# Optimization experiments

Hardware: AMD Instinct MI355X
Metric: run time of the kernel (lower is better)

Reference implementation:

```python
import jax, jax.numpy as jnp
import numpy as np

DET_COUNT = 729
N_ANGLES = 90
IMG = 512
FEATURES = 32
FILTER_SIZE = max(64, int(2 ** np.ceil(np.log2(2 * DET_COUNT))))  # 2048


def _ramp_filter(size):
    # scikit-image / torch_radon style spatial-domain ram-lak, then FFT
    n = np.concatenate([np.arange(1, size // 2 + 1, 2), np.arange(size // 2 - 1, 0, -2)])
    f = np.zeros(size, dtype=np.float64)
    f[0] = 0.25
    f[1::2] = -1.0 / (np.pi * n) ** 2
    return jnp.asarray(2.0 * np.real(np.fft.fft(f)), dtype=jnp.float32)

_RAMP = _ramp_filter(FILTER_SIZE)


def radon_forward(img, theta, det_count):
    # parallel-beam line integrals; img: (B, C, n, n)
    B, C, n, _ = img.shape
    c = (n - 1) / 2.0
    s = jnp.arange(det_count, dtype=img.dtype) - (det_count - 1) / 2.0  # detector offsets == ray steps
    cos, sin = jnp.cos(theta), jnp.sin(theta)
    # sample points: p = c + s*dir_perp + t*dir_ray   -> coords (A, D, T)
    px = c + s[None, :, None] * cos[:, None, None] - s[None, None, :] * sin[:, None, None]
    py = c + s[None, :, None] * sin[:, None, None] + s[None, None, :] * cos[:, None, None]

    def sample(im2d):
        vals = jax.scipy.ndimage.map_coordinates(im2d, [py, px], order=1, mode='constant', cval=0.0)
        return vals.sum(-1)  # integrate along ray -> (A, D)

    sino = jax.vmap(sample)(img.reshape(B * C, n, n))
    return sino.reshape(B, C, theta.shape[0], det_count)


def filter_sinogram(sino, n_angles):
    det = sino.shape[-1]
    padded = jnp.pad(sino, ((0, 0), (0, 0), (0, 0), (0, FILTER_SIZE - det)))
    out = jnp.real(jnp.fft.ifft(jnp.fft.fft(padded, axis=-1) * _RAMP, axis=-1))[..., :det]
    return out * (jnp.pi / (2.0 * n_angles))


def radon_backprojection(sino, theta, n):
    B, C, A, D = sino.shape
    c = (n - 1) / 2.0
    xs = jnp.arange(n, dtype=sino.dtype) - c
    X = xs[None, :]  # columns -> x
    Y = xs[:, None]  # rows    -> y
    cos, sin = jnp.cos(theta), jnp.sin(theta)
    pos = X[None] * cos[:, None, None] + Y[None] * sin[:, None, None] + (D - 1) / 2.0  # (A, n, n)
    i0 = jnp.clip(jnp.floor(pos), 0, D - 2).astype(jnp.int32)
    w = pos - i0
    valid = (pos >= 0) & (pos <= D - 1)

    def back_one(sino_ad):  # (A, D) -> (n, n)
        def per_angle(row, idx, ww, vv):
            v = row[idx] * (1.0 - ww) + row[idx + 1] * ww
            return jnp.where(vv, v, 0.0)
        return jax.vmap(per_angle)(sino_ad, i0, w, valid).sum(0)

    return jax.vmap(back_one)(sino.reshape(B * C, A, D)).reshape(B, C, n, n)


def conv2d(x, w):
    return jax.lax.conv_general_dilated(x, w, (1, 1), 'SAME', dimension_numbers=('NCHW', 'OIHW', 'NCHW'))


def setup_inputs():
    key = jax.random.key(0)
    ks = jax.random.split(key, 10)

    def xavier(k, shape):
        fan_in = shape[1] * shape[2] * shape[3]
        fan_out = shape[0] * shape[2] * shape[3]
        std = float(np.sqrt(2.0 / (fan_in + fan_out)))
        return jax.random.normal(k, shape, dtype=jnp.float32) * std

    x = jax.random.normal(ks[0], (1, 1, IMG, IMG), dtype=jnp.float32)
    theta = jnp.linspace(0.0, np.pi, N_ANGLES, endpoint=False).astype(jnp.float32)
    sinogram = jax.random.normal(ks[1], (1, 1, N_ANGLES, DET_COUNT), dtype=jnp.float32)
    return {
        'x': x, 'theta': theta, 'sinogram': sinogram,
        'lambda_step': jnp.asarray([0.5], dtype=jnp.float32),
        'soft_thr': jnp.asarray([0.01], dtype=jnp.float32),
        'conv_D': xavier(ks[2], (FEATURES, 1, 3, 3)),
        'conv1_forward': xavier(ks[3], (FEATURES, FEATURES, 3, 3)),
        'conv2_forward': xavier(ks[4], (FEATURES, FEATURES, 3, 3)),
        'conv1_backward': xavier(ks[5], (FEATURES, FEATURES, 3, 3)),
        'conv2_backward': xavier(ks[6], (FEATURES, FEATURES, 3, 3)),
        'conv_G': xavier(ks[7], (1, FEATURES, 3, 3)),
    }


def reference(x, theta, sinogram, lambda_step, soft_thr, conv_D, conv1_forward, conv2_forward, conv1_backward, conv2_backward, conv_G):
    sino_pred = radon_forward(x, theta, DET_COUNT)
    filtered = filter_sinogram(sino_pred, theta.shape[0])
    X_fbp = radon_backprojection(filtered - sinogram, theta, x.shape[2])
    x_input = x - lambda_step[0] * X_fbp

    x_D = conv2d(x_input, conv_D)
    h = jax.nn.relu(conv2d(x_D, conv1_forward))
    x_forward = conv2d(h, conv2_forward)
    st = jnp.sign(x_forward) * jax.nn.relu(jnp.abs(x_forward) - soft_thr[0])
    h = jax.nn.relu(conv2d(st, conv1_backward))
    x_backward = conv2d(h, conv2_backward)
    x_G = conv2d(x_backward, conv_G)
    x_pred = x_input + x_G

    h = jax.nn.relu(conv2d(x_forward, conv1_backward))
    x_D_est = conv2d(h, conv2_backward)
    symloss = x_D_est - x_D
    return (x_pred, symloss, symloss)
```

## Files before the change

### kernel.cpp

```cpp
#include <hip/hip_runtime.h>

#define IMG   512
#define NA    90
#define DET   729
#define NPIX  (IMG*IMG)
#define HW    514
#define QW    514
#define HBELEMS (HW*HW*32)

typedef __attribute__((ext_vector_type(8))) short     bf16x8;
typedef __attribute__((ext_vector_type(8))) unsigned short ushort8;
typedef __attribute__((ext_vector_type(4))) float     f32x4;

__device__ __forceinline__ unsigned short f2b(float f) {
    unsigned int u = __builtin_bit_cast(unsigned int, f);
    return (unsigned short)((u + 0x7FFFu + ((u >> 16) & 1u)) >> 16);
}
__device__ __forceinline__ float b2f(unsigned short h) {
    return __builtin_bit_cast(float, (unsigned int)h << 16);
}

__global__ void prep0_k(const float* __restrict__ theta, const float* __restrict__ img,
                        float* __restrict__ trig, float4* __restrict__ quad4,
                        float* __restrict__ sino) {
    if (blockIdx.x == 0) {
        int i = threadIdx.x;
        if (i < NA) {
            float t = theta[i];
            trig[2*i]   = cosf(t);
            trig[2*i+1] = sinf(t);
        }
        return;
    }
    if (blockIdx.x <= 1033) {
        int q = (blockIdx.x - 1) * 256 + threadIdx.x;
        if (q >= QW*QW) return;
        int qy = q / QW, qx = q - qy*QW;
        auto val = [&](int r, int c) -> float {
            return (r >= 1 && r <= 512 && c >= 1 && c <= 512) ? img[((r-1) << 9) + (c-1)] : 0.f;
        };
        quad4[q] = make_float4(val(qy, qx), val(qy, qx+1), val(qy+1, qx), val(qy+1, qx+1));
        return;
    }
    int z = (blockIdx.x - 1034) * 256 + threadIdx.x;
    if (z < NA*DET) sino[z] = 0.f;
}

__global__ __launch_bounds__(256) void radon_tile_k(const float4* __restrict__ quad4,
        const float* __restrict__ trig, float* __restrict__ sino) {
    __shared__ float4 tl4[1226];
    int b  = blockIdx.x;
    int tq = b % 289;
    int g  = b / 289;
    int tx = tq % 17, ty = tq / 17;
    int X0 = tx*32, Y0 = ty*32;
    int tid = threadIdx.x;

    for (int e = tid; e < 1226; e += 256) {
        float4 v = make_float4(0.f, 0.f, 0.f, 0.f);
        int r = e / 35, c = e - r*35;
        if (r >= 1 && r <= 32 && c >= 1 && c <= 32) {
            int gy = Y0 + r - 1, gx = X0 + c - 1;
            if (gy < QW && gx < QW) v = quad4[gy*QW + gx];
        }
        tl4[e] = v;
    }
    __syncthreads();

    int w = tid >> 6, lane = tid & 63;
    int a = g*4 + w;
    if (a >= NA) return;
    float cs = trig[2*a], sn = trig[2*a+1];

    float fX0 = (float)X0 - 1.0f;
    float fY0 = (float)Y0 - 1.0f;

    float cx0 = fX0 - 255.5f, cx1 = cx0 + 32.0f;
    float cy0 = fY0 - 255.5f, cy1 = cy0 + 32.0f;
    float sdmin = fminf(cx0*cs, cx1*cs) + fminf(cy0*sn, cy1*sn);
    float sdmax = fmaxf(cx0*cs, cx1*cs) + fmaxf(cy0*sn, cy1*sn);
    int dmin = (int)ceilf(sdmin + 364.0f) - 1; if (dmin < 0) dmin = 0;
    int dmax = (int)floorf(sdmax + 364.0f) + 1; if (dmax > DET-1) dmax = DET-1;
    int d = dmin + lane;
    if (d > dmax) return;

    float sd = (float)d - 364.0f;
    float bx = 255.5f + sd*cs, by = 255.5f + sd*sn;
    float lo = -365.0f, hi = 365.0f;
    if (sn > 1e-7f) {
        float inv = 1.0f / sn;
        lo = (bx - (fX0 + 32.0f)) * inv;
        hi = (bx - fX0) * inv;
    } else if (bx < fX0 || bx >= fX0 + 32.0f) return;
    if (fabsf(cs) > 1e-7f) {
        float inv = 1.0f / cs;
        float s1 = (fY0 - by) * inv, s2 = (fY0 + 32.0f - by) * inv;
        lo = fmaxf(lo, fminf(s1, s2));
        hi = fminf(hi, fmaxf(s1, s2));
    } else if (by < fY0 || by >= fY0 + 32.0f) return;
    int jlo = (int)ceilf(lo + 364.0f) - 1; if (jlo < 0) jlo = 0;
    int jhi = (int)floorf(hi + 364.0f) + 1; if (jhi > DET-1) jhi = DET-1;
    if (jlo > jhi) return;

    float sj = (float)jlo - 364.0f;
    float px2 = bx - sj*sn - fX0 + 1.0f;
    float py2 = by + sj*cs - fY0 + 1.0f;
    float acc = 0.f;
    #pragma unroll 2
    for (int j = jlo; j <= jhi; ++j) {
        float fpx = floorf(px2), fpy = floorf(py2);
        int ix = (int)fpx, iy = (int)fpy;
        float fx = px2 - fpx, fy = py2 - fpy;
        unsigned ba = ((unsigned)(iy*35 + ix)) * 16u;
        if (ba > 19584u) ba = 19600u;
        float4 q = *(const float4*)((const char*)tl4 + ba);
        float top = fmaf(fx, q.y - q.x, q.x);
        float bot = fmaf(fx, q.w - q.z, q.z);
        acc += fmaf(fy, bot - top, top);
        px2 -= sn; py2 += cs;
    }
    if (acc != 0.f) atomicAdd(&sino[a*DET + d], acc);
}

__global__ __launch_bounds__(768) void filter_k(const float* __restrict__ sino,
        const float* __restrict__ meas, float2* __restrict__ dpair) {
    __shared__ float prow[DET + 2*728];
    __shared__ float invsq[364];
    __shared__ float drow[DET];
    int a = blockIdx.x;
    for (int t = threadIdx.x; t < DET + 2*728; t += 768)
        prow[t] = (t >= 728 && t < 728 + DET) ? sino[a*DET + (t - 728)] : 0.f;
    const float cc = -2.0f / (3.14159265358979323846f * 3.14159265358979323846f);
    if (threadIdx.x < 364) {
        float dlt = (float)(2*threadIdx.x + 1);
        invsq[threadIdx.x] = cc / (dlt * dlt);
    }
    __syncthreads();
    const float scale = 3.14159265358979323846f / 180.0f;
    int i = threadIdx.x;
    if (i < DET) {
        const float* p = prow + 728 + i;
        float acc = 0.5f * p[0];
        #pragma unroll 4
        for (int k = 0; k < 364; k++) {
            int dlt = 2*k + 1;
            acc += (p[-dlt] + p[dlt]) * invsq[k];
        }
        drow[i] = acc * scale - meas[a*DET + i];
    }
    __syncthreads();
    if (i < DET)
        dpair[a*DET + i] = make_float2(drow[i], (i < DET-1) ? drow[i+1] : 0.f);
}

__global__ __launch_bounds__(256) void backproj_k(const float2* __restrict__ pair,
        const float* __restrict__ trig, const float* __restrict__ x,
        const float* __restrict__ lam, float* __restrict__ xin) {
    int pix = blockIdx.x * 256 + threadIdx.x;
    float X = (float)(pix & 511) - 255.5f;
    float Y = (float)(pix >> 9) - 255.5f;
    float acc = 0.f;
    for (int a = 0; a < NA; a++) {
        float pos = X*trig[2*a] + Y*trig[2*a+1] + 364.0f;
        if (pos >= 0.f && pos <= 728.f) {
            int i0 = (int)pos;
            if (i0 > 727) i0 = 727;
            float w = pos - (float)i0;
            float2 p = pair[a*DET + i0];
            acc += p.x + w*(p.y - p.x);
        }
    }
    xin[pix] = x[pix] - lam[0] * acc;
}

__global__ void prep1_k(unsigned short* __restrict__ hb0, size_t hbstride_elems,
                        const float* __restrict__ w0, const float* __restrict__ w1,
                        const float* __restrict__ w2, const float* __restrict__ w3,
                        const float* __restrict__ wg4,
                        unsigned short* __restrict__ wbuf) {
    int t = blockIdx.x * 256 + threadIdx.x;
    if (t < 4*2052) {
        int b = t / 2052, r = t - b*2052;
        int py, px;
        if      (r < 514)  { py = 0;            px = r; }
        else if (r < 1028) { py = 513;          px = r - 514; }
        else if (r < 1540) { py = r - 1028 + 1; px = 0; }
        else               { py = r - 1540 + 1; px = 513; }
        unsigned short* p = hb0 + b*hbstride_elems + ((size_t)py*HW + px)*32;
        uint4 z = make_uint4(0,0,0,0);
        ((uint4*)p)[0] = z; ((uint4*)p)[1] = z; ((uint4*)p)[2] = z; ((uint4*)p)[3] = z;
        return;
    }
    int tid = t - 4*2052;
    if (tid < 4*9216) {
        int L = tid / 9216, r = tid - L*9216;
        int tt = r >> 10, o = (r >> 5) & 31, i = r & 31;
        const float* s = (L == 0) ? w0 : (L == 1) ? w1 : (L == 2) ? w2 : w3;
        wbuf[tid] = f2b(s[o*288 + i*9 + tt]);
        return;
    }
    int gid = tid - 4*9216;
    if (gid >= 9*512) return;
    int tt = gid / 512, r = gid - tt*512;
    int o = r >> 5, i = r & 31;
    wbuf[4*9216 + gid] = (o == 0) ? f2b(wg4[i*9 + tt]) : (unsigned short)0;
}

__global__ __launch_bounds__(256) void convD_k(const float* __restrict__ xin,
        const float* __restrict__ wD, unsigned short* __restrict__ out_nhwc) {
    int pix = blockIdx.x * 256 + threadIdx.x;
    int y = pix >> 9, x = pix & 511;
    float v[9];
    #pragma unroll
    for (int dy = -1; dy <= 1; dy++)
        #pragma unroll
        for (int dx = -1; dx <= 1; dx++) {
            int yy = y + dy, xx = x + dx;
            v[(dy+1)*3 + dx+1] = (yy >= 0 && yy < 512 && xx >= 0 && xx < 512)
                                 ? xin[(yy << 9) + xx] : 0.f;
        }
    unsigned int packed[16];
    #pragma unroll
    for (int oc = 0; oc < 32; ++oc) {
        float acc = 0.f;
        #pragma unroll
        for (int t = 0; t < 9; t++) acc = fmaf(v[t], wD[oc*9 + t], acc);
        unsigned int b = f2b(acc);
        if (oc & 1) packed[oc >> 1] |= b << 16; else packed[oc >> 1] = b;
    }
    uint4* dst = (uint4*)(out_nhwc + ((size_t)(y+1)*HW + (x+1))*32);
    dst[0] = make_uint4(packed[0],  packed[1],  packed[2],  packed[3]);
    dst[1] = make_uint4(packed[4],  packed[5],  packed[6],  packed[7]);
    dst[2] = make_uint4(packed[8],  packed[9],  packed[10], packed[11]);
    dst[3] = make_uint4(packed[12], packed[13], packed[14], packed[15]);
}

template<int MODE>
__global__ __launch_bounds__(256, 4) void convM_k(const unsigned short* __restrict__ in,
        const unsigned short* __restrict__ wb,
        unsigned short* __restrict__ out0, unsigned short* __restrict__ out1,
        const float* __restrict__ thr_p,
        const unsigned short* __restrict__ aux, float* __restrict__ s1, float* __restrict__ s2) {
    int wv   = threadIdx.x >> 6;
    int lane = threadIdx.x & 63;
    int blk  = blockIdx.x;
    int xcd  = blk & 7;
    int idx  = blk >> 3;
    int by = (xcd << 2) + (idx >> 5);
    int bx = idx & 31;
    int x0 = bx*16;
    int yb = by*16 + wv*4;
    int lpix = lane & 15;
    int k8   = (lane >> 4) * 8;

    f32x4 acc[2][4];
    #pragma unroll
    for (int ob = 0; ob < 2; ob++)
        #pragma unroll
        for (int o = 0; o < 4; o++) acc[ob][o] = (f32x4){0.f,0.f,0.f,0.f};

    const short* base = (const short*)in + ((size_t)yb*HW + (x0 + lpix))*32 + k8;

    #pragma unroll
    for (int dx = 0; dx < 3; ++dx) {
        bf16x8 A2[3][2];
        #pragma unroll
        for (int dy = 0; dy < 3; ++dy)
            #pragma unroll
            for (int ob = 0; ob < 2; ob++)
                A2[dy][ob] = *(const bf16x8*)(wb + (dy*3+dx)*1024 + (ob*16 + lpix)*32 + k8);
        #pragma unroll
        for (int r = 0; r < 6; ++r) {
            bf16x8 B = *(const bf16x8*)(base + ((size_t)r*HW + dx)*32);
            #pragma unroll
            for (int dy = 0; dy < 3; ++dy) {
                int o = r - dy;
                if (o >= 0 && o < 4) {
                    acc[0][o] = __builtin_amdgcn_mfma_f32_16x16x32_bf16(A2[dy][0], B, acc[0][o], 0,0,0);
                    acc[1][o] = __builtin_amdgcn_mfma_f32_16x16x32_bf16(A2[dy][1], B, acc[1][o], 0,0,0);
                }
            }
        }
    }

    int prow = (lane >> 4) * 4;
    float thr = (MODE == 2) ? thr_p[0] : 0.f;
    #pragma unroll
    for (int ob = 0; ob < 2; ob++)
        #pragma unroll
        for (int o = 0; o < 4; o++) {
            f32x4 a = acc[ob][o];
            if (MODE == 3) {
                size_t aoff = ((size_t)(yb+o+1)*HW + (x0 + 1 + lpix))*32 + ob*16 + prow;
                ushort4 av = *(const ushort4*)(aux + aoff);
                int pix = ((yb+o) << 9) + x0 + lpix;
                float w0v = a[0] - b2f(av.x);
                float w1v = a[1] - b2f(av.y);
                float w2v = a[2] - b2f(av.z);
                float w3v = a[3] - b2f(av.w);
                int ocb = ob*16 + prow;
                s1[(size_t)(ocb+0)*NPIX + pix] = w0v; s2[(size_t)(ocb+0)*NPIX + pix] = w0v;
                s1[(size_t)(ocb+1)*NPIX + pix] = w1v; s2[(size_t)(ocb+1)*NPIX + pix] = w1v;
                s1[(size_t)(ocb+2)*NPIX + pix] = w2v; s2[(size_t)(ocb+2)*NPIX + pix] = w2v;
                s1[(size_t)(ocb+3)*NPIX + pix] = w3v; s2[(size_t)(ocb+3)*NPIX + pix] = w3v;
            } else {
                size_t off = ((size_t)(yb+o+1)*HW + (x0 + 1 + lpix))*32 + ob*16 + prow;
                if (MODE == 1) {
                    #pragma unroll
                    for (int r2 = 0; r2 < 4; r2++) a[r2] = fmaxf(a[r2], 0.f);
                }
                *(ushort4*)(out0 + off) = make_ushort4(f2b(a[0]), f2b(a[1]), f2b(a[2]), f2b(a[3]));
                if (MODE == 2) {
                    float st[4];
                    #pragma unroll
                    for (int r2 = 0; r2 < 4; r2++)
                        st[r2] = copysignf(fmaxf(fabsf(a[r2]) - thr, 0.f), a[r2]);
                    *(ushort4*)(out1 + off) = make_ushort4(f2b(st[0]), f2b(st[1]), f2b(st[2]), f2b(st[3]));
                }
            }
        }
}

__global__ __launch_bounds__(256) void convGM_k(const unsigned short* __restrict__ in,
        const unsigned short* __restrict__ wg,
        const float* __restrict__ xin, float* __restrict__ out) {
    int wid  = threadIdx.x >> 6;
    int lane = threadIdx.x & 63;
    int blk  = blockIdx.x;
    int xcd  = blk & 7;
    int idx  = blk >> 3;
    int by = (xcd << 4) + (idx >> 3);
    int bx = idx & 7;
    int y  = by*4 + wid;
    int x0 = bx*64;
    int lpix = lane & 15;
    int k8   = (lane >> 4) * 8;

    bf16x8 A[9];
    #pragma unroll
    for (int t = 0; t < 9; t++)
        A[t] = *(const bf16x8*)(wg + t*512 + lpix*32 + k8);

    f32x4 acc[4];
    #pragma unroll
    for (int p = 0; p < 4; p++) acc[p] = (f32x4){0.f,0.f,0.f,0.f};

    const short* base = (const short*)in + ((size_t)(y+1)*HW + (x0+1) + lpix)*32 + k8;
    #pragma unroll
    for (int dy = -1; dy <= 1; dy++)
        #pragma unroll
        for (int dx = -1; dx <= 1; dx++) {
            int t = (dy+1)*3 + (dx+1);
            const short* bp = base + (dy*HW + dx)*32;
            #pragma unroll
            for (int p = 0; p < 4; p++) {
                bf16x8 B = *(const bf16x8*)(bp + p*16*32);
                acc[p] = __builtin_amdgcn_mfma_f32_16x16x32_bf16(A[t], B, acc[p], 0,0,0);
            }
        }

    if (lane < 16) {
        #pragma unroll
        for (int p = 0; p < 4; p++) {
            int pix = (y << 9) + x0 + p*16 + lane;
            out[pix] = acc[p][0] + xin[pix];
        }
    }
}

extern "C" void kernel_launch(void* const* d_in, const int* in_sizes, int n_in,
                              void* d_out, int out_size, void* d_ws, size_t ws_size,
                              hipStream_t stream) {
    const float* x     = (const float*)d_in[0];
    const float* theta = (const float*)d_in[1];
    const float* meas  = (const float*)d_in[2];
    const float* lam   = (const float*)d_in[3];
    const float* thr   = (const float*)d_in[4];
    const float* wD    = (const float*)d_in[5];
    const float* w1f   = (const float*)d_in[6];
    const float* w2f   = (const float*)d_in[7];
    const float* w1b   = (const float*)d_in[8];
    const float* w2b   = (const float*)d_in[9];
    const float* wG    = (const float*)d_in[10];

    char* ws = (char*)d_ws;
    const size_t HBB = (size_t)HBELEMS * 2;
    unsigned short* HB1 = (unsigned short*)(ws);
    unsigned short* HB2 = (unsigned short*)(ws + HBB);
    unsigned short* HB3 = (unsigned short*)(ws + 2*HBB);
    unsigned short* HB4 = (unsigned short*)(ws + 3*HBB);
    float*  sino  = (float*)(ws + HBB);
    float2* dpair = (float2*)(ws + HBB + 524928);
    float4* quad4 = (float4*)(ws + 2*HBB);
    float* xin  = (float*)(ws + 4*HBB);
    float* trig = (float*)(ws + 4*HBB + 1048576);
    unsigned short* wbuf = (unsigned short*)(ws + 4*HBB + 1049600);
    unsigned short* wgbuf = wbuf + 4*9216;

    float* P  = (float*)d_out;
    float* S1 = P + NPIX;
    float* S2 = S1 + 32*NPIX;

    prep0_k<<<1 + 1033 + 257, 256, 0, stream>>>(theta, x, trig, quad4, sino);
    radon_tile_k<<<289*23, 256, 0, stream>>>(quad4, trig, sino);
    filter_k<<<NA, 768, 0, stream>>>(sino, meas, dpair);
    backproj_k<<<NPIX/256, 256, 0, stream>>>(dpair, trig, x, lam, xin);
    prep1_k<<<(4*2052 + 4*9216 + 9*512 + 255)/256, 256, 0, stream>>>(HB1, HBELEMS,
                                             w1f, w2f, w1b, w2b, wG, wbuf);

    convD_k<<<NPIX/256, 256, 0, stream>>>(xin, wD, HB1);
    convM_k<1><<<1024, 256, 0, stream>>>(HB1, wbuf + 0*9216, HB2, nullptr,
                                         nullptr, nullptr, nullptr, nullptr);
    convM_k<2><<<1024, 256, 0, stream>>>(HB2, wbuf + 1*9216, HB3, HB4,
                                         thr, nullptr, nullptr, nullptr);
    convM_k<1><<<1024, 256, 0, stream>>>(HB4, wbuf + 2*9216, HB2, nullptr,
                                         nullptr, nullptr, nullptr, nullptr);
    convM_k<0><<<1024, 256, 0, stream>>>(HB2, wbuf + 3*9216, HB4, nullptr,
                                         nullptr, nullptr, nullptr, nullptr);
    convGM_k<<<1024, 256, 0, stream>>>(HB4, wgbuf, xin, P);
    convM_k<1><<<1024, 256, 0, stream>>>(HB3, wbuf + 2*9216, HB2, nullptr,
                                         nullptr, nullptr, nullptr, nullptr);
    convM_k<3><<<1024, 256, 0, stream>>>(HB2, wbuf + 3*9216, nullptr, nullptr,
                                         nullptr, HB1, S1, S2);
}
```

Baseline: 213.0 us.

## Fuse consecutive 3x3 conv pairs through shared-memory halo tiles

Measured after the change: 234.0 us. +9.9%, slower.

```diff
diff --git a/kernel.cpp b/kernel.cpp
--- a/kernel.cpp
+++ b/kernel.cpp
@@ -4,9 +4,13 @@
 #define NA    90
 #define DET   729
 #define NPIX  (IMG*IMG)
-#define HW    514
+#define HW    516
 #define QW    514
 #define HBELEMS (HW*HW*32)
+
+#define ROWPX 34
+#define PIXB  80
+#define ROWB  (ROWPX*PIXB)
 
 typedef __attribute__((ext_vector_type(8))) short     bf16x8;
 typedef __attribute__((ext_vector_type(8))) unsigned short ushort8;
@@ -179,19 +183,25 @@
                         const float* __restrict__ wg4,
                         unsigned short* __restrict__ wbuf) {
     int t = blockIdx.x * 256 + threadIdx.x;
-    if (t < 4*2052) {
-        int b = t / 2052, r = t - b*2052;
+    if (t < 4*4112) {
+        int b = t / 4112, r = t - b*4112;
         int py, px;
-        if      (r < 514)  { py = 0;            px = r; }
-        else if (r < 1028) { py = 513;          px = r - 514; }
-        else if (r < 1540) { py = r - 1028 + 1; px = 0; }
-        else               { py = r - 1540 + 1; px = 513; }
+        if (r < 2064) {
+            int q = r / 516;
+            py = (q < 2) ? q : 512 + q;
+            px = r - q*516;
+        } else {
+            int rr = r - 2064;
+            int c = rr & 3;
+            px = (c < 2) ? c : 512 + c;
+            py = 2 + (rr >> 2);
+        }
         unsigned short* p = hb0 + b*hbstride_elems + ((size_t)py*HW + px)*32;
         uint4 z = make_uint4(0,0,0,0);
         ((uint4*)p)[0] = z; ((uint4*)p)[1] = z; ((uint4*)p)[2] = z; ((uint4*)p)[3] = z;
         return;
     }
-    int tid = t - 4*2052;
+    int tid = t - 4*4112;
     if (tid < 4*9216) {
         int L = tid / 9216, r = tid - L*9216;
         int tt = r >> 10, o = (r >> 5) & 31, i = r & 31;
@@ -228,7 +238,7 @@
         unsigned int b = f2b(acc);
         if (oc & 1) packed[oc >> 1] |= b << 16; else packed[oc >> 1] = b;
     }
-    uint4* dst = (uint4*)(out_nhwc + ((size_t)(y+1)*HW + (x+1))*32);
+    uint4* dst = (uint4*)(out_nhwc + ((size_t)(y+2)*HW + (x+2))*32);
     dst[0] = make_uint4(packed[0],  packed[1],  packed[2],  packed[3]);
     dst[1] = make_uint4(packed[4],  packed[5],  packed[6],  packed[7]);
     dst[2] = make_uint4(packed[8],  packed[9],  packed[10], packed[11]);
@@ -236,30 +246,136 @@
 }
 
 template<int MODE>
-__global__ __launch_bounds__(256, 4) void convM_k(const unsigned short* __restrict__ in,
-        const unsigned short* __restrict__ wb,
+__global__ __launch_bounds__(256, 3) void fusedM_k(const unsigned short* __restrict__ in,
+        const unsigned short* __restrict__ wbA, const unsigned short* __restrict__ wbB,
         unsigned short* __restrict__ out0, unsigned short* __restrict__ out1,
         const float* __restrict__ thr_p,
         const unsigned short* __restrict__ aux, float* __restrict__ s1, float* __restrict__ s2) {
+    __shared__ __align__(16) unsigned char smem[18*ROWB];
     int wv   = threadIdx.x >> 6;
     int lane = threadIdx.x & 63;
-    int blk  = blockIdx.x;
-    int xcd  = blk & 7;
-    int idx  = blk >> 3;
-    int by = (xcd << 2) + (idx >> 5);
-    int bx = idx & 31;
-    int x0 = bx*16;
-    int yb = by*16 + wv*4;
+    int bxi = blockIdx.x & 15, byi = blockIdx.x >> 4;
+    int xbase = bxi << 5;
+    int y0 = byi << 4;
     int lpix = lane & 15;
-    int k8   = (lane >> 4) * 8;
-
-    f32x4 acc[2][4];
+    int kg = lane >> 4;
+    int k8 = kg * 8;
+
+    int cb[3];
+    #pragma unroll
+    for (int g = 0; g < 3; g++) {
+        int c = xbase + g*16 + lpix;
+        cb[g] = c > 513 ? 513 : c;
+    }
+    const short* inb = (const short*)in + k8;
+
+    {
+        f32x4 acc[2][3][4];
+        #pragma unroll
+        for (int ob = 0; ob < 2; ob++)
+            #pragma unroll
+            for (int g = 0; g < 3; g++)
+                #pragma unroll
+                for (int o = 0; o < 4; o++) acc[ob][g][o] = (f32x4){0.f,0.f,0.f,0.f};
+
+        #pragma unroll
+        for (int dx = 0; dx < 3; ++dx) {
+            bf16x8 A2[3][2];
+            #pragma unroll
+            for (int dy = 0; dy < 3; ++dy)
+                #pragma unroll
+                for (int ob = 0; ob < 2; ob++)
+                    A2[dy][ob] = *(const bf16x8*)(wbA + (dy*3+dx)*1024 + (ob*16 + lpix)*32 + k8);
+            #pragma unroll
+            for (int r = 0; r < 6; ++r) {
+                size_t rowoff = (size_t)(y0 + 4*wv + r) * HW;
+                #pragma unroll
+                for (int g = 0; g < 3; ++g) {
+                    bf16x8 B = *(const bf16x8*)(inb + (rowoff + cb[g] + dx)*32);
+                    #pragma unroll
+                    for (int dy = 0; dy < 3; ++dy) {
+                        int o = r - dy;
+                        if (o >= 0 && o < 4) {
+                            acc[0][g][o] = __builtin_amdgcn_mfma_f32_16x16x32_bf16(A2[dy][0], B, acc[0][g][o], 0,0,0);
+                            acc[1][g][o] = __builtin_amdgcn_mfma_f32_16x16x32_bf16(A2[dy][1], B, acc[1][g][o], 0,0,0);
+                        }
+                    }
+                }
+            }
+        }
+        #pragma unroll
+        for (int g = 0; g < 3; ++g) {
+            int p = g*16 + lpix;
+            if (p < ROWPX) {
+                bool cok = ((unsigned)(xbase + p - 1)) < 512u;
+                #pragma unroll
+                for (int o = 0; o < 4; ++o) {
+                    int R = 4*wv + o;
+                    bool ok = cok && (((unsigned)(y0 + R - 1)) < 512u);
+                    #pragma unroll
+                    for (int ob = 0; ob < 2; ob++) {
+                        f32x4 a = acc[ob][g][o];
+                        ushort4 v = ok ? make_ushort4(f2b(fmaxf(a[0],0.f)), f2b(fmaxf(a[1],0.f)),
+                                                      f2b(fmaxf(a[2],0.f)), f2b(fmaxf(a[3],0.f)))
+                                       : make_ushort4(0,0,0,0);
+                        *(ushort4*)(smem + R*ROWB + p*PIXB + (ob*16 + kg*4)*2) = v;
+                    }
+                }
+            }
+        }
+    }
+    if (wv < 2) {
+        int R = 16 + wv;
+        f32x4 acc1[2][3];
+        #pragma unroll
+        for (int ob = 0; ob < 2; ob++)
+            #pragma unroll
+            for (int g = 0; g < 3; g++) acc1[ob][g] = (f32x4){0.f,0.f,0.f,0.f};
+        #pragma unroll
+        for (int dx = 0; dx < 3; ++dx) {
+            bf16x8 A2[3][2];
+            #pragma unroll
+            for (int dy = 0; dy < 3; ++dy)
+                #pragma unroll
+                for (int ob = 0; ob < 2; ob++)
+                    A2[dy][ob] = *(const bf16x8*)(wbA + (dy*3+dx)*1024 + (ob*16 + lpix)*32 + k8);
+            #pragma unroll
+            for (int dy = 0; dy < 3; ++dy) {
+                size_t rowoff = (size_t)(y0 + R + dy) * HW;
+                #pragma unroll
+                for (int g = 0; g < 3; ++g) {
+                    bf16x8 B = *(const bf16x8*)(inb + (rowoff + cb[g] + dx)*32);
+                    acc1[0][g] = __builtin_amdgcn_mfma_f32_16x16x32_bf16(A2[dy][0], B, acc1[0][g], 0,0,0);
+                    acc1[1][g] = __builtin_amdgcn_mfma_f32_16x16x32_bf16(A2[dy][1], B, acc1[1][g], 0,0,0);
+                }
+            }
+        }
+        bool rok = ((unsigned)(y0 + R - 1)) < 512u;
+        #pragma unroll
+        for (int g = 0; g < 3; ++g) {
+            int p = g*16 + lpix;
+            if (p < ROWPX) {
+                bool ok = rok && (((unsigned)(xbase + p - 1)) < 512u);
+                #pragma unroll
+                for (int ob = 0; ob < 2; ob++) {
+                    f32x4 a = acc1[ob][g];
+                    ushort4 v = ok ? make_ushort4(f2b(fmaxf(a[0],0.f)), f2b(fmaxf(a[1],0.f)),
+                                                  f2b(fmaxf(a[2],0.f)), f2b(fmaxf(a[3],0.f)))
+                                   : make_ushort4(0,0,0,0);
+                    *(ushort4*)(smem + R*ROWB + p*PIXB + (ob*16 + kg*4)*2) = v;
+                }
+            }
+        }
+    }
+    __syncthreads();
+
+    f32x4 acc2[2][2][4];
     #pragma unroll
     for (int ob = 0; ob < 2; ob++)
         #pragma unroll
-        for (int o = 0; o < 4; o++) acc[ob][o] = (f32x4){0.f,0.f,0.f,0.f};
-
-    const short* base = (const short*)in + ((size_t)yb*HW + (x0 + lpix))*32 + k8;
+        for (int g = 0; g < 2; g++)
+            #pragma unroll
+            for (int o = 0; o < 4; o++) acc2[ob][g][o] = (f32x4){0.f,0.f,0.f,0.f};
 
     #pragma unroll
     for (int dx = 0; dx < 3; ++dx) {
@@ -268,57 +384,59 @@
         for (int dy = 0; dy < 3; ++dy)
             #pragma unroll
             for (int ob = 0; ob < 2; ob++)
-                A2[dy][ob] = *(const bf16x8*)(wb + (dy*3+dx)*1024 + (ob*16 + lpix)*32 + k8);
+                A2[dy][ob] = *(const bf16x8*)(wbB + (dy*3+dx)*1024 + (ob*16 + lpix)*32 + k8);
         #pragma unroll
         for (int r = 0; r < 6; ++r) {
-            bf16x8 B = *(const bf16x8*)(base + ((size_t)r*HW + dx)*32);
-            #pragma unroll
-            for (int dy = 0; dy < 3; ++dy) {
-                int o = r - dy;
-                if (o >= 0 && o < 4) {
-                    acc[0][o] = __builtin_amdgcn_mfma_f32_16x16x32_bf16(A2[dy][0], B, acc[0][o], 0,0,0);
-                    acc[1][o] = __builtin_amdgcn_mfma_f32_16x16x32_bf16(A2[dy][1], B, acc[1][o], 0,0,0);
+            #pragma unroll
+            for (int g = 0; g < 2; ++g) {
+                bf16x8 B = *(const bf16x8*)(smem + (4*wv + r)*ROWB + (g*16 + lpix + dx)*PIXB + kg*16);
+                #pragma unroll
+                for (int dy = 0; dy < 3; ++dy) {
+                    int o = r - dy;
+                    if (o >= 0 && o < 4) {
+                        acc2[0][g][o] = __builtin_amdgcn_mfma_f32_16x16x32_bf16(A2[dy][0], B, acc2[0][g][o], 0,0,0);
+                        acc2[1][g][o] = __builtin_amdgcn_mfma_f32_16x16x32_bf16(A2[dy][1], B, acc2[1][g][o], 0,0,0);
+                    }
                 }
             }
         }
     }
 
-    int prow = (lane >> 4) * 4;
     float thr = (MODE == 2) ? thr_p[0] : 0.f;
     #pragma unroll
-    for (int ob = 0; ob < 2; ob++)
-        #pragma unroll
-        for (int o = 0; o < 4; o++) {
-            f32x4 a = acc[ob][o];
-            if (MODE == 3) {
-                size_t aoff = ((size_t)(yb+o+1)*HW + (x0 + 1 + lpix))*32 + ob*16 + prow;
-                ushort4 av = *(const ushort4*)(aux + aoff);
-                int pix = ((yb+o) << 9) + x0 + lpix;
-                float w0v = a[0] - b2f(av.x);
-                float w1v = a[1] - b2f(av.y);
-                float w2v = a[2] - b2f(av.z);
-                float w3v = a[3] - b2f(av.w);
-                int ocb = ob*16 + prow;
-                s1[(size_t)(ocb+0)*NPIX + pix] = w0v; s2[(size_t)(ocb+0)*NPIX + pix] = w0v;
-                s1[(size_t)(ocb+1)*NPIX + pix] = w1v; s2[(size_t)(ocb+1)*NPIX + pix] = w1v;
-                s1[(size_t)(ocb+2)*NPIX + pix] = w2v; s2[(size_t)(ocb+2)*NPIX + pix] = w2v;
-                s1[(size_t)(ocb+3)*NPIX + pix] = w3v; s2[(size_t)(ocb+3)*NPIX + pix] = w3v;
-            } else {
-                size_t off = ((size_t)(yb+o+1)*HW + (x0 + 1 + lpix))*32 + ob*16 + prow;
-                if (MODE == 1) {
-                    #pragma unroll
-                    for (int r2 = 0; r2 < 4; r2++) a[r2] = fmaxf(a[r2], 0.f);
+    for (int g = 0; g < 2; ++g)
+        #pragma unroll
+        for (int o = 0; o < 4; ++o)
+            #pragma unroll
+            for (int ob = 0; ob < 2; ob++) {
+                f32x4 a = acc2[ob][g][o];
+                int ox = xbase + g*16 + lpix;
+                int oy = y0 + 4*wv + o;
+                if (MODE == 3) {
+                    size_t aoff = ((size_t)(oy+2)*HW + (ox+2))*32 + ob*16 + kg*4;
+                    ushort4 av = *(const ushort4*)(aux + aoff);
+                    int pix = (oy << 9) + ox;
+                    float w0v = a[0] - b2f(av.x);
+                    float w1v = a[1] - b2f(av.y);
+                    float w2v = a[2] - b2f(av.z);
+                    float w3v = a[3] - b2f(av.w);
+                    int ocb = ob*16 + kg*4;
+                    s1[(size_t)(ocb+0)*NPIX + pix] = w0v; s2[(size_t)(ocb+0)*NPIX + pix] = w0v;
+                    s1[(size_t)(ocb+1)*NPIX + pix] = w1v; s2[(size_t)(ocb+1)*NPIX + pix] = w1v;
+                    s1[(size_t)(ocb+2)*NPIX + pix] = w2v; s2[(size_t)(ocb+2)*NPIX + pix] = w2v;
+                    s1[(size_t)(ocb+3)*NPIX + pix] = w3v; s2[(size_t)(ocb+3)*NPIX + pix] = w3v;
+                } else {
+                    size_t off = ((size_t)(oy+2)*HW + (ox+2))*32 + ob*16 + kg*4;
+                    *(ushort4*)(out0 + off) = make_ushort4(f2b(a[0]), f2b(a[1]), f2b(a[2]), f2b(a[3]));
+                    if (MODE == 2) {
+                        float st[4];
+                        #pragma unroll
+                        for (int r2 = 0; r2 < 4; r2++)
+                            st[r2] = copysignf(fmaxf(fabsf(a[r2]) - thr, 0.f), a[r2]);
+                        *(ushort4*)(out1 + off) = make_ushort4(f2b(st[0]), f2b(st[1]), f2b(st[2]), f2b(st[3]));
+                    }
                 }
-                *(ushort4*)(out0 + off) = make_ushort4(f2b(a[0]), f2b(a[1]), f2b(a[2]), f2b(a[3]));
-                if (MODE == 2) {
-                    float st[4];
-                    #pragma unroll
-                    for (int r2 = 0; r2 < 4; r2++)
-                        st[r2] = copysignf(fmaxf(fabsf(a[r2]) - thr, 0.f), a[r2]);
-                    *(ushort4*)(out1 + off) = make_ushort4(f2b(st[0]), f2b(st[1]), f2b(st[2]), f2b(st[3]));
-                }
-            }
-        }
+            }
 }
 
 __global__ __launch_bounds__(256) void convGM_k(const unsigned short* __restrict__ in,
@@ -345,7 +463,7 @@
     #pragma unroll
     for (int p = 0; p < 4; p++) acc[p] = (f32x4){0.f,0.f,0.f,0.f};
 
-    const short* base = (const short*)in + ((size_t)(y+1)*HW + (x0+1) + lpix)*32 + k8;
+    const short* base = (const short*)in + ((size_t)(y+2)*HW + (x0+2) + lpix)*32 + k8;
     #pragma unroll
     for (int dy = -1; dy <= 1; dy++)
         #pragma unroll
@@ -405,21 +523,15 @@
     radon_tile_k<<<289*23, 256, 0, stream>>>(quad4, trig, sino);
     filter_k<<<NA, 768, 0, stream>>>(sino, meas, dpair);
     backproj_k<<<NPIX/256, 256, 0, stream>>>(dpair, trig, x, lam, xin);
-    prep1_k<<<(4*2052 + 4*9216 + 9*512 + 255)/256, 256, 0, stream>>>(HB1, HBELEMS,
+    prep1_k<<<(4*4112 + 4*9216 + 9*512 + 255)/256, 256, 0, stream>>>(HB1, HBELEMS,
                                              w1f, w2f, w1b, w2b, wG, wbuf);
 
     convD_k<<<NPIX/256, 256, 0, stream>>>(xin, wD, HB1);
-    convM_k<1><<<1024, 256, 0, stream>>>(HB1, wbuf + 0*9216, HB2, nullptr,
-                                         nullptr, nullptr, nullptr, nullptr);
-    convM_k<2><<<1024, 256, 0, stream>>>(HB2, wbuf + 1*9216, HB3, HB4,
-                                         thr, nullptr, nullptr, nullptr);
-    convM_k<1><<<1024, 256, 0, stream>>>(HB4, wbuf + 2*9216, HB2, nullptr,
-                                         nullptr, nullptr, nullptr, nullptr);
-    convM_k<0><<<1024, 256, 0, stream>>>(HB2, wbuf + 3*9216, HB4, nullptr,
-                                         nullptr, nullptr, nullptr, nullptr);
-    convGM_k<<<1024, 256, 0, stream>>>(HB4, wgbuf, xin, P);
-    convM_k<1><<<1024, 256, 0, stream>>>(HB3, wbuf + 2*9216, HB2, nullptr,
-                                         nullptr, nullptr, nullptr, nullptr);
-    convM_k<3><<<1024, 256, 0, stream>>>(HB2, wbuf + 3*9216, nullptr, nullptr,
-                                         nullptr, HB1, S1, S2);
-}
+    fusedM_k<2><<<512, 256, 0, stream>>>(HB1, wbuf + 0*9216, wbuf + 1*9216,
+                                         HB3, HB4, thr, nullptr, nullptr, nullptr);
+    fusedM_k<0><<<512, 256, 0, stream>>>(HB4, wbuf + 2*9216, wbuf + 3*9216,
+                                         HB2, nullptr, nullptr, nullptr, nullptr, nullptr);
+    convGM_k<<<1024, 256, 0, stream>>>(HB2, wgbuf, xin, P);
+    fusedM_k<3><<<512, 256, 0, stream>>>(HB3, wbuf + 2*9216, wbuf + 3*9216,
+                                         nullptr, nullptr, nullptr, HB1, S1, S2);
+}
```
